# Optimization experiments

Measured on AMD Instinct MI355X. Metric: run time of the kernel, lower is better.

The kernel has to match this reference:

```python
import jax, jax.numpy as jnp
import numpy as np


def setup_inputs() -> dict:
    key = jax.random.key(0)
    ks = jax.random.split(key, 6)
    B, T, S, D, H, V = 8, 256, 512, 768, 8, 32000
    return {
        "dec_output": jax.random.normal(ks[0], (B, T, D), dtype=jnp.float32),
        "final_output": jax.random.normal(ks[1], (B, T, V), dtype=jnp.float32),
        "attention_weights": jax.random.normal(ks[2], (B, H, T, S), dtype=jnp.float32),
        "encoder_input": jax.random.randint(ks[3], (B, S), 0, V, dtype=jnp.int32),
        "W": jax.random.normal(ks[4], (D, 1), dtype=jnp.float32) * 0.02,
        "b": jnp.zeros((1,), dtype=jnp.float32),
        "inp_shape": S,
        "tar_shape": T,
        "batch": B,
        "training": 0,
    }


def reference(dec_output, final_output, attention_weights, encoder_input, W, b,
              inp_shape, tar_shape, batch, training):
    B, T, V = final_output.shape
    # p_gen: Dense(1, sigmoid) on decoder output -> [B, T, 1]
    p_gen = jax.nn.sigmoid(jnp.einsum("btd,do->bto", dec_output, W) + b)
    # vocab distribution scaled by p_gen
    vocab_dist = p_gen * jax.nn.softmax(final_output, axis=-1)  # [B, T, V]
    # mean over heads, softmax over source positions -> [B, T, S]
    attention_dist = jax.nn.softmax(jnp.mean(attention_weights, axis=1), axis=-1)
    updates = (1.0 - p_gen) * attention_dist  # [B, T, S]
    # scatter-add attention mass onto source token ids in vocab space
    b_idx = jnp.arange(B)[:, None, None]           # [B,1,1]
    t_idx = jnp.arange(T)[None, :, None]           # [1,T,1]
    v_idx = encoder_input[:, None, :]              # [B,1,S]
    copy_probs = jnp.zeros((B, T, V), dtype=vocab_dist.dtype).at[
        b_idx, t_idx, v_idx].add(updates)
    combined_logits = jnp.log(vocab_dist + copy_probs + 0.001)
    return combined_logits
```

## Files before the change

kernel.cpp:

```cpp
#include <hip/hip_runtime.h>
#include <stdint.h>

#define B_ 8
#define T_ 256
#define S_ 512
#define D_ 768
#define H_ 8
#define V_ 32000
#define BLOCK 512
#define NWAVE (BLOCK / 64)
#define NF4 (V_ / 4)
#define SLOTS 1024
#define EMPTYK 0xFFFFFFFFu
#define BMW ((V_ + 31) / 32)

typedef float vf4 __attribute__((ext_vector_type(4)));

static __device__ __forceinline__ float e4(vf4 v) {
    return __expf(v.x) + __expf(v.y) + __expf(v.z) + __expf(v.w);
}

__global__ __launch_bounds__(BLOCK, 8) void ptrgen_f32(
    const float* __restrict__ dec,
    const float* __restrict__ fin,
    const float* __restrict__ attw,
    const int* __restrict__ enc,
    const float* __restrict__ W,
    const float* __restrict__ bbias,
    float* __restrict__ out)
{
    __shared__ unsigned int hkey[SLOTS];
    __shared__ float        hval[SLOTS];
    __shared__ unsigned int bmap[BMW];
    __shared__ float sred[3 * NWAVE];
    __shared__ float sbc[3];

    const int tid = threadIdx.x;
    const int bid = blockIdx.x;
    const int b = bid >> 8;
    const int t = bid & 255;

#pragma unroll
    for (int i = tid; i < SLOTS; i += BLOCK) { hkey[i] = EMPTYK; hval[i] = 0.0f; }
    for (int i = tid; i < BMW; i += BLOCK) bmap[i] = 0u;

    float pp = dec[(size_t)bid * D_ + tid] * W[tid];
    if (tid < D_ - BLOCK)
        pp += dec[(size_t)bid * D_ + BLOCK + tid] * W[BLOCK + tid];

    const float* ab = attw + ((size_t)(b * H_) * T_ + t) * S_ + tid;
    float s = 0.0f;
#pragma unroll
    for (int h = 0; h < H_; ++h) s += ab[(size_t)h * (T_ * S_)];
    const float ae = __expf(s * (1.0f / H_));
    const int token = enc[b * S_ + tid];

    __syncthreads();

    atomicOr(&bmap[token >> 5], 1u << (token & 31));
    {
        unsigned int h = ((unsigned int)token * 2654435761u) >> 22;
        for (;;) {
            unsigned int prev = atomicCAS(&hkey[h], EMPTYK, (unsigned int)token);
            if (prev == EMPTYK || prev == (unsigned int)token) {
                atomicAdd(&hval[h], ae);
                break;
            }
            h = (h + 1) & (SLOTS - 1);
        }
    }

    const vf4* rowf = (const vf4*)(fin + (size_t)bid * V_);
    float lsum = 0.0f;
#pragma unroll 5
    for (int i = 0; i < 15; ++i) lsum += e4(rowf[tid + i * BLOCK]);
    if (tid < NF4 - 15 * BLOCK)
        lsum += e4(rowf[tid + 15 * BLOCK]);

    const int lane = tid & 63, wid = tid >> 6;
    float v0 = pp, v1 = ae, v2 = lsum;
#pragma unroll
    for (int o = 32; o; o >>= 1) {
        v0 += __shfl_xor(v0, o, 64);
        v1 += __shfl_xor(v1, o, 64);
        v2 += __shfl_xor(v2, o, 64);
    }
    if (lane == 0) {
        sred[wid] = v0;
        sred[NWAVE + wid] = v1;
        sred[2 * NWAVE + wid] = v2;
    }
    __syncthreads();
    if (wid == 0) {
        float a0 = (lane < NWAVE) ? sred[lane] : 0.0f;
        float a1 = (lane < NWAVE) ? sred[NWAVE + lane] : 0.0f;
        float a2 = (lane < NWAVE) ? sred[2 * NWAVE + lane] : 0.0f;
#pragma unroll
        for (int o = 4; o; o >>= 1) {
            a0 += __shfl_xor(a0, o, 64);
            a1 += __shfl_xor(a1, o, 64);
            a2 += __shfl_xor(a2, o, 64);
        }
        if (lane == 0) { sbc[0] = a0; sbc[1] = a1; sbc[2] = a2; }
    }
    __syncthreads();

    const float p_gen  = 1.0f / (1.0f + __expf(-(sbc[0] + bbias[0])));
    const float inv_l  = p_gen / sbc[2];
    const float cscale = (1.0f - p_gen) / sbc[1];

    vf4* outp = (vf4*)(out + (size_t)bid * V_);

    auto hget = [&](int idx) -> float {
        unsigned int h = ((unsigned int)idx * 2654435761u) >> 22;
        for (;;) {
            unsigned int k = hkey[h];
            if (k == (unsigned int)idx) return hval[h];
            if (k == EMPTYK) return 0.0f;
            h = (h + 1) & (SLOTS - 1);
        }
    };

#pragma unroll 4
    for (int c = tid; c < NF4; c += BLOCK) {
        const vf4 x = __builtin_nontemporal_load(rowf + c);
        const unsigned int nib = (bmap[c >> 3] >> ((c & 7) * 4)) & 0xFu;
        float c0 = 0.0f, c1 = 0.0f, c2 = 0.0f, c3 = 0.0f;
        if (nib) {
            if (nib & 1u) c0 = hget(4 * c + 0);
            if (nib & 2u) c1 = hget(4 * c + 1);
            if (nib & 4u) c2 = hget(4 * c + 2);
            if (nib & 8u) c3 = hget(4 * c + 3);
        }
        vf4 y;
        y.x = __logf(fmaf(__expf(x.x), inv_l, fmaf(c0, cscale, 0.001f)));
        y.y = __logf(fmaf(__expf(x.y), inv_l, fmaf(c1, cscale, 0.001f)));
        y.z = __logf(fmaf(__expf(x.z), inv_l, fmaf(c2, cscale, 0.001f)));
        y.w = __logf(fmaf(__expf(x.w), inv_l, fmaf(c3, cscale, 0.001f)));
        __builtin_nontemporal_store(y, outp + c);
    }
}

extern "C" void kernel_launch(void* const* d_in, const int* in_sizes, int n_in,
                              void* d_out, int out_size, void* d_ws, size_t ws_size,
                              hipStream_t stream) {
    const float* dec   = (const float*)d_in[0];
    const float* fin   = (const float*)d_in[1];
    const float* attw  = (const float*)d_in[2];
    const int*   enc   = (const int*)d_in[3];
    const float* W     = (const float*)d_in[4];
    const float* bbias = (const float*)d_in[5];
    float* out = (float*)d_out;

    ptrgen_f32<<<B_ * T_, BLOCK, 0, stream>>>(dec, fin, attw, enc, W, bbias, out);
}
```

Measured before the change: 492.3 us.

## Keep each row in registers and software-pipeline eight rows per block

Each 1024-thread block now handles eight consecutive (b,t) rows. The final_output row is held in registers, so it is read from global memory once instead of twice (once for the softmax sum, once for the output). The next row's logits, attention and decoder values are prefetched while the current row is reduced and written. A triple-buffered shared hash table lets the next row's scatter run alongside the current row's lookups. The trade-off is heavy register pressure (16 vf4 per thread), fewer resident blocks and a grid of only 256 blocks.

```diff
diff --git a/kernel.cpp b/kernel.cpp
--- a/kernel.cpp
+++ b/kernel.cpp
@@ -7,20 +7,34 @@
 #define D_ 768
 #define H_ 8
 #define V_ 32000
-#define BLOCK 512
+#define BLOCK 1024
 #define NWAVE (BLOCK / 64)
 #define NF4 (V_ / 4)
+#define TAIL (NF4 - 7 * BLOCK)
+#define ROWS 8
+#define GRID (B_ * T_ / ROWS)
 #define SLOTS 1024
 #define EMPTYK 0xFFFFFFFFu
 #define BMW ((V_ + 31) / 32)
 
 typedef float vf4 __attribute__((ext_vector_type(4)));
 
-static __device__ __forceinline__ float e4(vf4 v) {
-    return __expf(v.x) + __expf(v.y) + __expf(v.z) + __expf(v.w);
+struct LBuf {
+    unsigned int hkey[SLOTS];
+    float        hval[SLOTS];
+    unsigned int bmap[BMW];
+};
+
+static __device__ __forceinline__ vf4 expv(vf4 v) {
+    vf4 r;
+    r.x = __expf(v.x);
+    r.y = __expf(v.y);
+    r.z = __expf(v.z);
+    r.w = __expf(v.w);
+    return r;
 }
 
-__global__ __launch_bounds__(BLOCK, 8) void ptrgen_f32(
+__global__ __launch_bounds__(BLOCK, 4) void ptrgen_f32(
     const float* __restrict__ dec,
     const float* __restrict__ fin,
     const float* __restrict__ attw,
@@ -29,115 +43,175 @@
     const float* __restrict__ bbias,
     float* __restrict__ out)
 {
-    __shared__ unsigned int hkey[SLOTS];
-    __shared__ float        hval[SLOTS];
-    __shared__ unsigned int bmap[BMW];
+    __shared__ LBuf lb[3];
     __shared__ float sred[3 * NWAVE];
     __shared__ float sbc[3];
 
     const int tid = threadIdx.x;
-    const int bid = blockIdx.x;
-    const int b = bid >> 8;
-    const int t = bid & 255;
-
-#pragma unroll
-    for (int i = tid; i < SLOTS; i += BLOCK) { hkey[i] = EMPTYK; hval[i] = 0.0f; }
-    for (int i = tid; i < BMW; i += BLOCK) bmap[i] = 0u;
-
-    float pp = dec[(size_t)bid * D_ + tid] * W[tid];
-    if (tid < D_ - BLOCK)
-        pp += dec[(size_t)bid * D_ + BLOCK + tid] * W[BLOCK + tid];
-
-    const float* ab = attw + ((size_t)(b * H_) * T_ + t) * S_ + tid;
-    float s = 0.0f;
-#pragma unroll
-    for (int h = 0; h < H_; ++h) s += ab[(size_t)h * (T_ * S_)];
-    const float ae = __expf(s * (1.0f / H_));
-    const int token = enc[b * S_ + tid];
-
+    const int base = blockIdx.x * ROWS;
+    const int b = base >> 8;
+    const int lane = tid & 63, wid = tid >> 6;
+    const bool isS = tid < S_;
+    const bool isD = tid < D_;
+    const bool hasT = tid < TAIL;
+
+    const float Wv = isD ? W[tid] : 0.0f;
+    const int token = isS ? enc[b * S_ + tid] : 0;
+    const float bb = bbias[0];
+    const unsigned int hash0 = ((unsigned int)token * 2654435761u) >> 22;
+
+    float pp_c = 0.0f, ae_c = 0.0f;
+    if (isD) pp_c = dec[(size_t)base * D_ + tid] * Wv;
+    if (isS) {
+        const float* ab = attw + ((size_t)(b * H_) * T_ + (base & 255)) * S_ + tid;
+        float s = 0.0f;
+#pragma unroll
+        for (int h = 0; h < H_; ++h) s += ab[(size_t)h * (T_ * S_)];
+        ae_c = __expf(s * (1.0f / H_));
+    }
+    for (int k = tid; k < SLOTS; k += BLOCK) { lb[0].hkey[k] = EMPTYK; lb[0].hval[k] = 0.0f; }
+    for (int k = tid; k < BMW; k += BLOCK) lb[0].bmap[k] = 0u;
     __syncthreads();
-
-    atomicOr(&bmap[token >> 5], 1u << (token & 31));
+    if (isS) {
+        atomicOr(&lb[0].bmap[token >> 5], 1u << (token & 31));
+        unsigned int h = hash0;
+        for (;;) {
+            unsigned int prev = atomicCAS(&lb[0].hkey[h], EMPTYK, (unsigned int)token);
+            if (prev == EMPTYK || prev == (unsigned int)token) { atomicAdd(&lb[0].hval[h], ae_c); break; }
+            h = (h + 1) & (SLOTS - 1);
+        }
+    }
+
+    vf4 Areg[8], Breg[8];
     {
-        unsigned int h = ((unsigned int)token * 2654435761u) >> 22;
-        for (;;) {
-            unsigned int prev = atomicCAS(&hkey[h], EMPTYK, (unsigned int)token);
-            if (prev == EMPTYK || prev == (unsigned int)token) {
-                atomicAdd(&hval[h], ae);
-                break;
-            }
-            h = (h + 1) & (SLOTS - 1);
-        }
-    }
-
-    const vf4* rowf = (const vf4*)(fin + (size_t)bid * V_);
-    float lsum = 0.0f;
-#pragma unroll 5
-    for (int i = 0; i < 15; ++i) lsum += e4(rowf[tid + i * BLOCK]);
-    if (tid < NF4 - 15 * BLOCK)
-        lsum += e4(rowf[tid + 15 * BLOCK]);
-
-    const int lane = tid & 63, wid = tid >> 6;
-    float v0 = pp, v1 = ae, v2 = lsum;
-#pragma unroll
-    for (int o = 32; o; o >>= 1) {
-        v0 += __shfl_xor(v0, o, 64);
-        v1 += __shfl_xor(v1, o, 64);
-        v2 += __shfl_xor(v2, o, 64);
-    }
-    if (lane == 0) {
-        sred[wid] = v0;
-        sred[NWAVE + wid] = v1;
-        sred[2 * NWAVE + wid] = v2;
-    }
-    __syncthreads();
-    if (wid == 0) {
-        float a0 = (lane < NWAVE) ? sred[lane] : 0.0f;
-        float a1 = (lane < NWAVE) ? sred[NWAVE + lane] : 0.0f;
-        float a2 = (lane < NWAVE) ? sred[2 * NWAVE + lane] : 0.0f;
-#pragma unroll
-        for (int o = 4; o; o >>= 1) {
-            a0 += __shfl_xor(a0, o, 64);
-            a1 += __shfl_xor(a1, o, 64);
-            a2 += __shfl_xor(a2, o, 64);
-        }
-        if (lane == 0) { sbc[0] = a0; sbc[1] = a1; sbc[2] = a2; }
-    }
-    __syncthreads();
-
-    const float p_gen  = 1.0f / (1.0f + __expf(-(sbc[0] + bbias[0])));
-    const float inv_l  = p_gen / sbc[2];
-    const float cscale = (1.0f - p_gen) / sbc[1];
-
-    vf4* outp = (vf4*)(out + (size_t)bid * V_);
-
-    auto hget = [&](int idx) -> float {
-        unsigned int h = ((unsigned int)idx * 2654435761u) >> 22;
-        for (;;) {
-            unsigned int k = hkey[h];
-            if (k == (unsigned int)idx) return hval[h];
-            if (k == EMPTYK) return 0.0f;
-            h = (h + 1) & (SLOTS - 1);
-        }
+        const vf4* rowf = (const vf4*)(fin + (size_t)base * V_);
+#pragma unroll
+        for (int j = 0; j < 7; ++j) Areg[j] = __builtin_nontemporal_load(rowf + tid + j * BLOCK);
+        Areg[7] = hasT ? __builtin_nontemporal_load(rowf + tid + 7 * BLOCK) : (vf4)(0.0f);
+    }
+
+    float pp_n = 0.0f, ae_n = 0.0f;
+
+    auto body = [&](int i, vf4* CUR, vf4* NXT) {
+        const int row = base + i;
+        const bool more = (i < ROWS - 1);
+
+        float aw[8] = {0, 0, 0, 0, 0, 0, 0, 0};
+        float dv = 0.0f;
+        if (more) {
+            if (isS) {
+                const float* ab = attw + ((size_t)(b * H_) * T_ + ((row + 1) & 255)) * S_ + tid;
+#pragma unroll
+                for (int h = 0; h < H_; ++h) aw[h] = ab[(size_t)h * (T_ * S_)];
+            }
+            if (isD) dv = dec[(size_t)(row + 1) * D_ + tid];
+        }
+
+        float lsum = 0.0f;
+#pragma unroll
+        for (int j = 0; j < 7; ++j) {
+            CUR[j] = expv(CUR[j]);
+            lsum += CUR[j].x + CUR[j].y + CUR[j].z + CUR[j].w;
+        }
+        if (hasT) {
+            CUR[7] = expv(CUR[7]);
+            lsum += CUR[7].x + CUR[7].y + CUR[7].z + CUR[7].w;
+        } else {
+            CUR[7] = (vf4)(0.0f);
+        }
+
+        LBuf* zb = &lb[(i + 1) % 3];
+        for (int k = tid; k < SLOTS; k += BLOCK) { zb->hkey[k] = EMPTYK; zb->hval[k] = 0.0f; }
+        for (int k = tid; k < BMW; k += BLOCK) zb->bmap[k] = 0u;
+
+        float v0 = pp_c, v1 = ae_c, v2 = lsum;
+#pragma unroll
+        for (int o = 32; o; o >>= 1) {
+            v0 += __shfl_xor(v0, o, 64);
+            v1 += __shfl_xor(v1, o, 64);
+            v2 += __shfl_xor(v2, o, 64);
+        }
+        if (lane == 0) { sred[wid] = v0; sred[NWAVE + wid] = v1; sred[2 * NWAVE + wid] = v2; }
+        __syncthreads();
+        if (wid == 0) {
+            float a0 = (lane < NWAVE) ? sred[lane] : 0.0f;
+            float a1 = (lane < NWAVE) ? sred[NWAVE + lane] : 0.0f;
+            float a2 = (lane < NWAVE) ? sred[2 * NWAVE + lane] : 0.0f;
+#pragma unroll
+            for (int o = 8; o; o >>= 1) {
+                a0 += __shfl_xor(a0, o, 64);
+                a1 += __shfl_xor(a1, o, 64);
+                a2 += __shfl_xor(a2, o, 64);
+            }
+            if (lane == 0) { sbc[0] = a0; sbc[1] = a1; sbc[2] = a2; }
+        }
+        __syncthreads();
+
+        const float p_gen  = 1.0f / (1.0f + __expf(-(sbc[0] + bb)));
+        const float inv_l  = p_gen / sbc[2];
+        const float cscale = (1.0f - p_gen) / sbc[1];
+
+        if (more) {
+            const vf4* rowf = (const vf4*)(fin + (size_t)(row + 1) * V_);
+#pragma unroll
+            for (int j = 0; j < 7; ++j) NXT[j] = __builtin_nontemporal_load(rowf + tid + j * BLOCK);
+            NXT[7] = hasT ? __builtin_nontemporal_load(rowf + tid + 7 * BLOCK) : (vf4)(0.0f);
+            pp_n = isD ? dv * Wv : 0.0f;
+            if (isS) {
+                float s = aw[0] + aw[1] + aw[2] + aw[3] + aw[4] + aw[5] + aw[6] + aw[7];
+                ae_n = __expf(s * (1.0f / H_));
+                atomicOr(&zb->bmap[token >> 5], 1u << (token & 31));
+                unsigned int h = hash0;
+                for (;;) {
+                    unsigned int prev = atomicCAS(&zb->hkey[h], EMPTYK, (unsigned int)token);
+                    if (prev == EMPTYK || prev == (unsigned int)token) { atomicAdd(&zb->hval[h], ae_n); break; }
+                    h = (h + 1) & (SLOTS - 1);
+                }
+            } else {
+                ae_n = 0.0f;
+            }
+        }
+
+        LBuf* eb = &lb[i % 3];
+        vf4* outp = (vf4*)(out + (size_t)row * V_);
+        auto hget = [&](int idx) -> float {
+            unsigned int h = ((unsigned int)idx * 2654435761u) >> 22;
+            for (;;) {
+                unsigned int k = eb->hkey[h];
+                if (k == (unsigned int)idx) return eb->hval[h];
+                if (k == EMPTYK) return 0.0f;
+                h = (h + 1) & (SLOTS - 1);
+            }
+        };
+#pragma unroll
+        for (int j = 0; j < 8; ++j) {
+            if (j < 7 || hasT) {
+                const int c = tid + j * BLOCK;
+                const vf4 e = CUR[j];
+                const unsigned int nib = (eb->bmap[c >> 3] >> ((c & 7) * 4)) & 0xFu;
+                float c0 = 0.0f, c1 = 0.0f, c2 = 0.0f, c3 = 0.0f;
+                if (nib) {
+                    if (nib & 1u) c0 = hget(4 * c + 0);
+                    if (nib & 2u) c1 = hget(4 * c + 1);
+                    if (nib & 4u) c2 = hget(4 * c + 2);
+                    if (nib & 8u) c3 = hget(4 * c + 3);
+                }
+                vf4 y;
+                y.x = __logf(fmaf(e.x, inv_l, fmaf(c0, cscale, 0.001f)));
+                y.y = __logf(fmaf(e.y, inv_l, fmaf(c1, cscale, 0.001f)));
+                y.z = __logf(fmaf(e.z, inv_l, fmaf(c2, cscale, 0.001f)));
+                y.w = __logf(fmaf(e.w, inv_l, fmaf(c3, cscale, 0.001f)));
+                __builtin_nontemporal_store(y, outp + c);
+            }
+        }
+        pp_c = pp_n;
+        ae_c = ae_n;
     };
 
-#pragma unroll 4
-    for (int c = tid; c < NF4; c += BLOCK) {
-        const vf4 x = __builtin_nontemporal_load(rowf + c);
-        const unsigned int nib = (bmap[c >> 3] >> ((c & 7) * 4)) & 0xFu;
-        float c0 = 0.0f, c1 = 0.0f, c2 = 0.0f, c3 = 0.0f;
-        if (nib) {
-            if (nib & 1u) c0 = hget(4 * c + 0);
-            if (nib & 2u) c1 = hget(4 * c + 1);
-            if (nib & 4u) c2 = hget(4 * c + 2);
-            if (nib & 8u) c3 = hget(4 * c + 3);
-        }
-        vf4 y;
-        y.x = __logf(fmaf(__expf(x.x), inv_l, fmaf(c0, cscale, 0.001f)));
-        y.y = __logf(fmaf(__expf(x.y), inv_l, fmaf(c1, cscale, 0.001f)));
-        y.z = __logf(fmaf(__expf(x.z), inv_l, fmaf(c2, cscale, 0.001f)));
-        y.w = __logf(fmaf(__expf(x.w), inv_l, fmaf(c3, cscale, 0.001f)));
-        __builtin_nontemporal_store(y, outp + c);
+#pragma unroll
+    for (int ii = 0; ii < ROWS; ii += 2) {
+        body(ii, Areg, Breg);
+        body(ii + 1, Breg, Areg);
     }
 }
 
@@ -152,5 +226,5 @@
     const float* bbias = (const float*)d_in[5];
     float* out = (float*)d_out;
 
-    ptrgen_f32<<<B_ * T_, BLOCK, 0, stream>>>(dec, fin, attw, enc, W, bbias, out);
+    ptrgen_f32<<<GRID, BLOCK, 0, stream>>>(dec, fin, attw, enc, W, bbias, out);
 }
```

After: 568.3 us. 15.4% more time.
